# Kernel tuning notes

Hardware: AMD Instinct MI355X
Metric: run time of the kernel (lower is better)

The kernel has to match this reference:

```python
import jax, jax.numpy as jnp
import numpy as np

B, S, D, H, OUT = 512, 200, 64, 512, 1
EPS = 1e-5  # torch LayerNorm default


def ln(x, g, b, axes=-1):
    m = x.mean(axis=axes, keepdims=True)
    v = ((x - m) ** 2).mean(axis=axes, keepdims=True)
    return (x - m) * jax.lax.rsqrt(v + EPS) * g + b


def lstm_layer(xs, W_ih, b_ih, W_hh, b_hh, g_ih, be_ih, g_hh, be_hh, g_ho, be_ho):
    # xs: (S, B, in_dim) -> (S, B, H)
    nb = xs.shape[1]
    def step(carry, x_t):
        h, c = carry
        gates = ln(x_t @ W_ih.T + b_ih, g_ih, be_ih) + ln(h @ W_hh.T + b_hh, g_hh, be_hh)
        i, f, g, o = jnp.split(gates, 4, axis=-1)
        c_new = jax.nn.sigmoid(f) * c + jax.nn.sigmoid(i) * jnp.tanh(g)
        h_new = jax.nn.sigmoid(o) * ln(jnp.tanh(c_new), g_ho, be_ho)
        return (h_new, c_new), h_new
    init = (jnp.zeros((nb, H), xs.dtype), jnp.zeros((nb, H), xs.dtype))
    _, hs = jax.lax.scan(step, init, xs)
    return hs


def setup_inputs() -> dict:
    key = jax.random.key(0)
    ks = iter(jax.random.split(key, 16))
    scale = 0.02
    def rn(shape):
        return jax.random.normal(next(ks), shape, jnp.float32) * scale
    inp = {"x": jax.random.normal(next(ks), (B, S, D), jnp.float32)}
    inp["ln1_g"] = jnp.ones((S, D), jnp.float32)
    inp["ln1_b"] = jnp.zeros((S, D), jnp.float32)
    for l, ind in ((0, D), (1, H)):
        inp[f"W_ih{l}"] = rn((4 * H, ind)); inp[f"b_ih{l}"] = jnp.zeros((4 * H,), jnp.float32)
        inp[f"W_hh{l}"] = rn((4 * H, H));  inp[f"b_hh{l}"] = jnp.zeros((4 * H,), jnp.float32)
        inp[f"g_ih{l}"] = jnp.ones((4 * H,), jnp.float32); inp[f"be_ih{l}"] = jnp.zeros((4 * H,), jnp.float32)
        inp[f"g_hh{l}"] = jnp.ones((4 * H,), jnp.float32); inp[f"be_hh{l}"] = jnp.zeros((4 * H,), jnp.float32)
        inp[f"g_ho{l}"] = jnp.ones((H,), jnp.float32);     inp[f"be_ho{l}"] = jnp.zeros((H,), jnp.float32)
    inp["Wd1"] = rn((H // 4, H));      inp["bd1"] = jnp.zeros((H // 4,), jnp.float32)
    inp["Wd2"] = rn((H // 8, H // 4)); inp["bd2"] = jnp.zeros((H // 8,), jnp.float32)
    inp["Wd3"] = rn((H // 16, H // 8)); inp["bd3"] = jnp.zeros((H // 16,), jnp.float32)
    inp["Wd4"] = rn((OUT, H // 16));   inp["bd4"] = jnp.zeros((OUT,), jnp.float32)
    return inp


def _forward(x, ln1_g, ln1_b,
             W_ih0, b_ih0, W_hh0, b_hh0, g_ih0, be_ih0, g_hh0, be_hh0, g_ho0, be_ho0,
             W_ih1, b_ih1, W_hh1, b_hh1, g_ih1, be_ih1, g_hh1, be_hh1, g_ho1, be_ho1,
             Wd1, bd1, Wd2, bd2, Wd3, bd3, Wd4, bd4):
    # ln1 normalizes jointly over (seq_len, input_dim)
    x = ln(x, ln1_g, ln1_b, axes=(-2, -1))
    xs = jnp.transpose(x, (1, 0, 2))  # (S, B, D)
    hs = lstm_layer(xs, W_ih0, b_ih0, W_hh0, b_hh0, g_ih0, be_ih0, g_hh0, be_hh0, g_ho0, be_ho0)
    hs = lstm_layer(hs, W_ih1, b_ih1, W_hh1, b_hh1, g_ih1, be_ih1, g_hh1, be_hh1, g_ho1, be_ho1)
    h_last = hs[-1]  # (B, H): last_num=1, eval-mode dropout is identity
    z = jax.nn.relu(h_last @ Wd1.T + bd1)
    z = jax.nn.relu(z @ Wd2.T + bd2)
    z = jax.nn.relu(z @ Wd3.T + bd3)
    return z @ Wd4.T + bd4  # (B, OUT)


def reference(x, ln1_g, ln1_b,
              W_ih0, b_ih0, W_hh0, b_hh0, g_ih0, be_ih0, g_hh0, be_hh0, g_ho0, be_ho0,
              W_ih1, b_ih1, W_hh1, b_hh1, g_ih1, be_ih1, g_hh1, be_hh1, g_ho1, be_ho1,
              Wd1, bd1, Wd2, bd2, Wd3, bd3, Wd4, bd4):
    return _forward(x, ln1_g, ln1_b,
                    W_ih0, b_ih0, W_hh0, b_hh0, g_ih0, be_ih0, g_hh0, be_hh0, g_ho0, be_ho0,
                    W_ih1, b_ih1, W_hh1, b_hh1, g_ih1, be_ih1, g_hh1, be_hh1, g_ho1, be_ho1,
                    Wd1, bd1, Wd2, bd2, Wd3, bd3, Wd4, bd4)
```

## Files before the change

### kernel.cpp

```cpp
#include <hip/hip_runtime.h>
#include <math.h>

#define BATCH 512
#define SEQ   200
#define DIN   64
#define HID   512
#define GW    2048
#define EPS   1e-5f
#define NREG  4

typedef _Float16 half_t;
typedef half_t half8 __attribute__((ext_vector_type(8)));
typedef float  f32x4  __attribute__((ext_vector_type(4)));
typedef float  f32x16 __attribute__((ext_vector_type(16)));

#define WN0 (2048*64)
#define WN1 (2048*512)
#define WTOT (WN0 + 3*WN1)
#define XFRAG ((size_t)SEQ*16*4*512)

__device__ __forceinline__ float sigf(float x){ return 1.0f/(1.0f+expf(-x)); }

__device__ __forceinline__ void block_reduce4(float&a,float&b,float&c,float&d,float* red){
  #pragma unroll
  for(int o=32;o;o>>=1){
    a+=__shfl_down(a,o); b+=__shfl_down(b,o);
    c+=__shfl_down(c,o); d+=__shfl_down(d,o);
  }
  const int lane = threadIdx.x & 63, wid = threadIdx.x>>6;
  if(lane==0){ red[wid*4+0]=a; red[wid*4+1]=b; red[wid*4+2]=c; red[wid*4+3]=d; }
  __syncthreads();
  a = red[0]+red[4]+red[8]+red[12];
  b = red[1]+red[5]+red[9]+red[13];
  c = red[2]+red[6]+red[10]+red[14];
  d = red[3]+red[7]+red[11]+red[15];
  __syncthreads();
}

__global__ __launch_bounds__(256) void ln1_stats(const float* __restrict__ x,
                                                 float* __restrict__ mu,
                                                 float* __restrict__ rs){
  const int b = blockIdx.x;
  const float* xb = x + (size_t)b*SEQ*DIN;
  float s=0, ss=0, d=0, e=0;
  for (int i=threadIdx.x; i<SEQ*DIN; i+=256){ float v=xb[i]; s+=v; ss+=v*v; }
  __shared__ float red[16];
  block_reduce4(s,ss,d,e,red);
  if (threadIdx.x==0){
    float m = s*(1.0f/(SEQ*DIN));
    mu[b] = m;
    rs[b] = rsqrtf(ss*(1.0f/(SEQ*DIN)) - m*m + EPS);
  }
}

__global__ __launch_bounds__(256) void wsplit(
    const float* __restrict__ W0, const float* __restrict__ W1,
    const float* __restrict__ W2, const float* __restrict__ W3,
    half_t* __restrict__ Wh, half_t* __restrict__ Wl)
{
  int i = blockIdx.x*256 + threadIdx.x;
  if (i >= WTOT) return;
  const float* src; int off, Kd;
  if (i < WN0){ src=W0; off=i; Kd=DIN; }
  else {
    int r = (i-WN0)/WN1; off = (i-WN0) - r*WN1; Kd=HID;
    src = (r==0)?W1:((r==1)?W2:W3);
  }
  const int C = Kd>>5;
  int j  = off & 7;
  int l  = (off>>3) & 63;
  int ks = (off>>9) & 1;
  int nf = (off>>10) & 1;
  int pc = off>>11;
  int c  = pc & (C-1);
  int p  = pc >> (Kd==DIN ? 1 : 4);
  int n  = p*64 + nf*32 + (l&31);
  int k  = c*32 + ks*16 + (l>>5)*8 + j;
  float v = src[(size_t)n*Kd + k];
  half_t h = (half_t)v;
  Wh[i] = h;
  Wl[i] = (half_t)(v - (float)h);
}

__global__ __launch_bounds__(256) void xprep(
    const float* __restrict__ x, const float* __restrict__ g1, const float* __restrict__ b1,
    const float* __restrict__ mu, const float* __restrict__ rs,
    half_t* __restrict__ xh, half_t* __restrict__ xl)
{
  size_t i = (size_t)blockIdx.x*256 + threadIdx.x;
  if (i >= XFRAG) return;
  int j   = (int)(i & 7);
  int l   = (int)((i>>3) & 63);
  int c   = (int)((i>>9) & 3);
  int mch = (int)((i>>11) & 15);
  int t   = (int)(i>>15);
  int b   = mch*32 + (l&31);
  int k   = c*16 + ((l>>5)<<3) + j;
  float v = (x[(size_t)b*(SEQ*DIN) + t*DIN + k] - mu[b]) * rs[b]
            * g1[t*DIN+k] + b1[t*DIN+k];
  half_t h = (half_t)v;
  xh[i] = h;
  xl[i] = (half_t)(v - (float)h);
}

__global__ __launch_bounds__(256, 1) void tick_mm64(
    const half_t* __restrict__ xh, const half_t* __restrict__ xl,
    const half_t* __restrict__ h0fh, const half_t* __restrict__ h0fl,
    const half_t* __restrict__ h1fh, const half_t* __restrict__ h1fl,
    const half_t* __restrict__ Wh, const half_t* __restrict__ Wl,
    float* __restrict__ G, int t)
{
  const int z    = blockIdx.z;
  const int tid  = threadIdx.x;
  const int lane = tid & 63;
  const int w    = tid >> 6;
  const int ln31 = lane & 31;

  const int mch0 = blockIdx.y*2;
  const int p    = blockIdx.x*4 + w;
  const int wn0  = p*64;

  const half_t* Bh = Wh + WN0; const half_t* Bl = Wl + WN0;
  int Kd = HID;
  if (z==0){ Bh=Wh; Bl=Wl; Kd=DIN; }
  else if (z==2){ Bh=Wh+WN0+WN1; Bl=Wl+WN0+WN1; }
  else if (z==3){ Bh=Wh+WN0+2*WN1; Bl=Wl+WN0+2*WN1; }

  const int C32 = Kd >> 5;
  const int C16 = Kd >> 4;

  const half_t* Bph = Bh + (size_t)p*C32*2048 + lane*8;
  const half_t* Bpl = Bl + (size_t)p*C32*2048 + lane*8;

  const int tq = (t < SEQ) ? t : (SEQ-1);
  const half_t *Aph0,*Apl0,*Aph1,*Apl1;
  if (z==0){
    const size_t xb = ((size_t)tq*16 + mch0)*2048 + lane*8;
    Aph0 = xh + xb; Aph1 = xh + xb + 2048;
    Apl0 = xl + xb; Apl1 = xl + xb + 2048;
  } else {
    const half_t* FAh = (z==3) ? h1fh : h0fh;
    const half_t* FAl = (z==3) ? h1fl : h0fl;
    const size_t ab = (size_t)mch0*16384 + lane*8;
    Aph0 = FAh + ab; Aph1 = FAh + ab + 16384;
    Apl0 = FAl + ab; Apl1 = FAl + ab + 16384;
  }

  f32x16 acc00 = {0.f,0.f,0.f,0.f,0.f,0.f,0.f,0.f,0.f,0.f,0.f,0.f,0.f,0.f,0.f,0.f};
  f32x16 acc01 = acc00, acc10 = acc00, acc11 = acc00;

  struct F { half8 ah0,al0,ah1,al1,bh0,bh1,bl0,bl1; };
  auto loadF = [&](int c)->F{
    F f;
    const size_t ao = (size_t)c*512;
    f.ah0 = *(const half8*)(Aph0 + ao);
    f.al0 = *(const half8*)(Apl0 + ao);
    f.ah1 = *(const half8*)(Aph1 + ao);
    f.al1 = *(const half8*)(Apl1 + ao);
    const size_t bo = (size_t)(c>>1)*2048 + (size_t)(c&1)*512;
    f.bh0 = *(const half8*)(Bph + bo);
    f.bh1 = *(const half8*)(Bph + bo + 1024);
    f.bl0 = *(const half8*)(Bpl + bo);
    f.bl1 = *(const half8*)(Bpl + bo + 1024);
    return f;
  };
  auto mmstep = [&](const F& f){
    acc00 = __builtin_amdgcn_mfma_f32_32x32x16_f16(f.ah0, f.bh0, acc00, 0,0,0);
    acc01 = __builtin_amdgcn_mfma_f32_32x32x16_f16(f.ah0, f.bh1, acc01, 0,0,0);
    acc10 = __builtin_amdgcn_mfma_f32_32x32x16_f16(f.ah1, f.bh0, acc10, 0,0,0);
    acc11 = __builtin_amdgcn_mfma_f32_32x32x16_f16(f.ah1, f.bh1, acc11, 0,0,0);
    acc00 = __builtin_amdgcn_mfma_f32_32x32x16_f16(f.al0, f.bh0, acc00, 0,0,0);
    acc01 = __builtin_amdgcn_mfma_f32_32x32x16_f16(f.al0, f.bh1, acc01, 0,0,0);
    acc10 = __builtin_amdgcn_mfma_f32_32x32x16_f16(f.al1, f.bh0, acc10, 0,0,0);
    acc11 = __builtin_amdgcn_mfma_f32_32x32x16_f16(f.al1, f.bh1, acc11, 0,0,0);
    acc00 = __builtin_amdgcn_mfma_f32_32x32x16_f16(f.ah0, f.bl0, acc00, 0,0,0);
    acc01 = __builtin_amdgcn_mfma_f32_32x32x16_f16(f.ah0, f.bl1, acc01, 0,0,0);
    acc10 = __builtin_amdgcn_mfma_f32_32x32x16_f16(f.ah1, f.bl0, acc10, 0,0,0);
    acc11 = __builtin_amdgcn_mfma_f32_32x32x16_f16(f.ah1, f.bl1, acc11, 0,0,0);
  };

  F f0 = loadF(0);
  F f1 = loadF(1);
  for (int c=0; c<C16; c+=2){
    F f2, f3;
    if (c+2 < C16){ f2 = loadF(c+2); f3 = loadF(c+3); }
    mmstep(f0);
    mmstep(f1);
    f0 = f2; f1 = f3;
  }

  float* Gr = G + (size_t)z*BATCH*GW;
  const int rbase = (lane>>5)<<2;
  #pragma unroll
  for (int reg=0; reg<16; reg++){
    const int row = (reg&3) + ((reg>>2)<<3) + rbase;
    const int m0 = mch0*32 + row;
    const int m1 = m0 + 32;
    __builtin_nontemporal_store(acc00[reg], &Gr[(size_t)m0*GW + wn0 + ln31]);
    __builtin_nontemporal_store(acc01[reg], &Gr[(size_t)m0*GW + wn0 + 32 + ln31]);
    __builtin_nontemporal_store(acc10[reg], &Gr[(size_t)m1*GW + wn0 + ln31]);
    __builtin_nontemporal_store(acc11[reg], &Gr[(size_t)m1*GW + wn0 + 32 + ln31]);
  }
}

__global__ __launch_bounds__(256) void tick_update(
    const float* __restrict__ G,
    const float* __restrict__ b_ih0, const float* __restrict__ b_hh0,
    const float* __restrict__ b_ih1, const float* __restrict__ b_hh1,
    const float* __restrict__ g_ih0, const float* __restrict__ be_ih0,
    const float* __restrict__ g_hh0, const float* __restrict__ be_hh0,
    const float* __restrict__ g_ho0, const float* __restrict__ be_ho0,
    const float* __restrict__ g_ih1, const float* __restrict__ be_ih1,
    const float* __restrict__ g_hh1, const float* __restrict__ be_hh1,
    const float* __restrict__ g_ho1, const float* __restrict__ be_ho1,
    float* __restrict__ h0, float* __restrict__ c0,
    float* __restrict__ h1, float* __restrict__ c1,
    half_t* __restrict__ h0fh, half_t* __restrict__ h0fl,
    half_t* __restrict__ h1fh, half_t* __restrict__ h1fl, int t)
{
  const int layer = blockIdx.x >> 9;
  const int b = blockIdx.x & 511;
  if (layer==0 && t>=SEQ) return;
  if (layer==1 && t==0)   return;

  const float *GA,*GB,*bA,*bB,*gA,*beA,*gB,*beB,*gH,*bH;
  float *cs,*hs; half_t *hfx,*lfx;
  const size_t rb = (size_t)b*GW;
  if (layer==0){
    GA = G + rb;
    GB = G + (size_t)1*BATCH*GW + rb;
    bA=b_ih0; bB=b_hh0;
    gA=g_ih0; beA=be_ih0; gB=g_hh0; beB=be_hh0; gH=g_ho0; bH=be_ho0;
    cs = c0 + b*HID; hs = h0 + b*HID; hfx = h0fh; lfx = h0fl;
  } else {
    GA = G + (size_t)2*BATCH*GW + rb;
    GB = G + (size_t)3*BATCH*GW + rb;
    bA=b_ih1; bB=b_hh1;
    gA=g_ih1; beA=be_ih1; gB=g_hh1; beB=be_hh1; gH=g_ho1; bH=be_ho1;
    cs = c1 + b*HID; hs = h1 + b*HID; hfx = h1fh; lfx = h1fl;
  }

  const int tid = threadIdx.x;
  __shared__ float red[16];
  __shared__ __align__(16) float GS[2*GW];
  __shared__ float su[HID];
  __shared__ float so[HID];

  float sa=0, ssa=0, sb=0, ssb=0;
  for (int i=tid*4; i<GW; i+=1024){
    f32x4 va = *(const f32x4*)(GA+i);
    va += *(const f32x4*)(bA+i);
    *(f32x4*)(GS+i) = va;
    f32x4 vb = *(const f32x4*)(GB+i);
    vb += *(const f32x4*)(bB+i);
    *(f32x4*)(GS+GW+i) = vb;
    #pragma unroll
    for (int q=0;q<4;q++){
      sa += va[q]; ssa += va[q]*va[q];
      sb += vb[q]; ssb += vb[q]*vb[q];
    }
  }
  block_reduce4(sa,ssa,sb,ssb,red);
  const float ma = sa*(1.0f/GW);
  const float ra = rsqrtf(ssa*(1.0f/GW) - ma*ma + EPS);
  const float mb = sb*(1.0f/GW);
  const float rb_ = rsqrtf(ssb*(1.0f/GW) - mb*mb + EPS);

  float s_u=0, s_uu=0;
  for (int j=tid;j<HID;j+=256){
    float iv = ((GS[j      ]-ma)*ra*gA[j      ]+beA[j      ]) + ((GS[GW+j      ]-mb)*rb_*gB[j      ]+beB[j      ]);
    float fv = ((GS[j+  HID]-ma)*ra*gA[j+  HID]+beA[j+  HID]) + ((GS[GW+j+  HID]-mb)*rb_*gB[j+  HID]+beB[j+  HID]);
    float gv = ((GS[j+2*HID]-ma)*ra*gA[j+2*HID]+beA[j+2*HID]) + ((GS[GW+j+2*HID]-mb)*rb_*gB[j+2*HID]+beB[j+2*HID]);
    float ov = ((GS[j+3*HID]-ma)*ra*gA[j+3*HID]+beA[j+3*HID]) + ((GS[GW+j+3*HID]-mb)*rb_*gB[j+3*HID]+beB[j+3*HID]);
    float cn = sigf(fv)*cs[j] + sigf(iv)*tanhf(gv);
    cs[j] = cn;
    float u = tanhf(cn);
    su[j] = u; so[j] = sigf(ov);
    s_u += u; s_uu += u*u;
  }
  float d3=0,d4=0;
  block_reduce4(s_u,s_uu,d3,d4,red);
  const float mu_u = s_u*(1.0f/HID);
  const float ru   = rsqrtf(s_uu*(1.0f/HID) - mu_u*mu_u + EPS);

  const size_t fbase = ((size_t)(b>>5)*32)*512 + (size_t)(b&31)*8;
  for (int j=tid;j<HID;j+=256){
    float v = so[j] * ((su[j]-mu_u)*ru*gH[j] + bH[j]);
    hs[j] = v;
    half_t hv = (half_t)v;
    half_t lv = (half_t)(v - (float)hv);
    const size_t fi = fbase + (size_t)(j>>4)*512 + (size_t)((j>>3)&1)*256 + (j&7);
    hfx[fi] = hv;
    lfx[fi] = lv;
  }
}

__global__ __launch_bounds__(256) void head_kernel(
    const float* __restrict__ h1,
    const float* __restrict__ Wd1, const float* __restrict__ bd1,
    const float* __restrict__ Wd2, const float* __restrict__ bd2,
    const float* __restrict__ Wd3, const float* __restrict__ bd3,
    const float* __restrict__ Wd4, const float* __restrict__ bd4,
    float* __restrict__ out)
{
  const int b = blockIdx.x;
  __shared__ float hv[HID];
  __shared__ float z1[128];
  __shared__ float z2[64];
  __shared__ float z3[32];
  const int tid = threadIdx.x;
  for (int i=tid;i<HID;i+=256) hv[i]=h1[(size_t)b*HID+i];
  __syncthreads();
  if (tid<128){
    float acc=bd1[tid]; const float* w=Wd1+(size_t)tid*512;
    for(int k=0;k<512;k++) acc+=hv[k]*w[k];
    z1[tid]=fmaxf(acc,0.f);
  }
  __syncthreads();
  if (tid<64){
    float acc=bd2[tid]; const float* w=Wd2+(size_t)tid*128;
    for(int k=0;k<128;k++) acc+=z1[k]*w[k];
    z2[tid]=fmaxf(acc,0.f);
  }
  __syncthreads();
  if (tid<32){
    float acc=bd3[tid]; const float* w=Wd3+(size_t)tid*64;
    for(int k=0;k<64;k++) acc+=z2[k]*w[k];
    z3[tid]=fmaxf(acc,0.f);
  }
  __syncthreads();
  if (tid==0){
    float acc=bd4[0];
    for(int k=0;k<32;k++) acc+=z3[k]*Wd4[k];
    out[b]=acc;
  }
}

extern "C" void kernel_launch(void* const* d_in, const int* in_sizes, int n_in,
                              void* d_out, int out_size, void* d_ws, size_t ws_size,
                              hipStream_t stream) {
  const float* x      = (const float*)d_in[0];
  const float* ln1_g  = (const float*)d_in[1];
  const float* ln1_b  = (const float*)d_in[2];
  const float* W_ih0  = (const float*)d_in[3];
  const float* b_ih0  = (const float*)d_in[4];
  const float* W_hh0  = (const float*)d_in[5];
  const float* b_hh0  = (const float*)d_in[6];
  const float* g_ih0  = (const float*)d_in[7];
  const float* be_ih0 = (const float*)d_in[8];
  const float* g_hh0  = (const float*)d_in[9];
  const float* be_hh0 = (const float*)d_in[10];
  const float* g_ho0  = (const float*)d_in[11];
  const float* be_ho0 = (const float*)d_in[12];
  const float* W_ih1  = (const float*)d_in[13];
  const float* b_ih1  = (const float*)d_in[14];
  const float* W_hh1  = (const float*)d_in[15];
  const float* b_hh1  = (const float*)d_in[16];
  const float* g_ih1  = (const float*)d_in[17];
  const float* be_ih1 = (const float*)d_in[18];
  const float* g_hh1  = (const float*)d_in[19];
  const float* be_hh1 = (const float*)d_in[20];
  const float* g_ho1  = (const float*)d_in[21];
  const float* be_ho1 = (const float*)d_in[22];
  const float* Wd1    = (const float*)d_in[23];
  const float* bd1    = (const float*)d_in[24];
  const float* Wd2    = (const float*)d_in[25];
  const float* bd2    = (const float*)d_in[26];
  const float* Wd3    = (const float*)d_in[27];
  const float* bd3    = (const float*)d_in[28];
  const float* Wd4    = (const float*)d_in[29];
  const float* bd4    = (const float*)d_in[30];
  float* out = (float*)d_out;

  float* ws = (float*)d_ws;
  float* G  = ws;
  float* h0 = G  + NREG*(size_t)BATCH*GW;
  float* c0 = h0 + (size_t)BATCH*HID;
  float* h1 = c0 + (size_t)BATCH*HID;
  float* c1 = h1 + (size_t)BATCH*HID;
  half_t* h0fh = (half_t*)(c1 + (size_t)BATCH*HID);
  half_t* h0fl = h0fh + (size_t)BATCH*HID;
  half_t* h1fh = h0fl + (size_t)BATCH*HID;
  half_t* h1fl = h1fh + (size_t)BATCH*HID;
  float* mu = (float*)(h1fl + (size_t)BATCH*HID);
  float* rs = mu + BATCH;
  half_t* Wh = (half_t*)(rs + BATCH);
  half_t* Wl = Wh + (size_t)WTOT;
  half_t* xh = Wl + (size_t)WTOT;
  half_t* xl = xh + XFRAG;

  hipMemsetAsync(h0, 0, 4*(size_t)BATCH*HID*4 + 4*(size_t)BATCH*HID*2, stream);

  ln1_stats<<<BATCH, 256, 0, stream>>>(x, mu, rs);
  wsplit<<<(WTOT+255)/256, 256, 0, stream>>>(W_ih0, W_hh0, W_ih1, W_hh1, Wh, Wl);
  xprep<<<(int)((XFRAG+255)/256), 256, 0, stream>>>(x, ln1_g, ln1_b, mu, rs, xh, xl);

  dim3 mgrid(8, 8, NREG);
  for (int t = 0; t <= SEQ; ++t) {
    tick_mm64<<<mgrid, 256, 0, stream>>>(xh, xl,
        h0fh, h0fl, h1fh, h1fl, Wh, Wl, G, t);
    tick_update<<<dim3(1024), 256, 0, stream>>>(G,
        b_ih0, b_hh0, b_ih1, b_hh1,
        g_ih0, be_ih0, g_hh0, be_hh0, g_ho0, be_ho0,
        g_ih1, be_ih1, g_hh1, be_hh1, g_ho1, be_ho1,
        h0, c0, h1, c1, h0fh, h0fl, h1fh, h1fl, t);
  }
  head_kernel<<<BATCH, 256, 0, stream>>>(h1, Wd1, bd1, Wd2, bd2, Wd3, bd3, Wd4, bd4, out);
}
```

Before: 5.677 ms.

## Fuse matmul and update phases into staggered combined kernels with double-buffered h0

The per-tick matmul and LSTM-update kernels are merged into a single 'phase' kernel that runs matmul blocks for one layer alongside update blocks for the other layer, skewing the two layers in time. Layer-0 hidden fragments are double-buffered by parity so layer-1 matmuls can read the previous h0 while layer-0 updates write the next. This puts GEMM and elementwise work in the same launch so they can share the GPU, at the cost of 640-block launches, a different dependency schedule and extra buffers. G reads also switch to nontemporal loads.

New measurement: 7.288 ms. 28.4% more time.

```diff
diff --git a/kernel.cpp b/kernel.cpp
--- a/kernel.cpp
+++ b/kernel.cpp
@@ -18,6 +18,7 @@
 #define WN1 (2048*512)
 #define WTOT (WN0 + 3*WN1)
 #define XFRAG ((size_t)SEQ*16*4*512)
+#define HFRAG ((size_t)BATCH*HID)
 
 __device__ __forceinline__ float sigf(float x){ return 1.0f/(1.0f+expf(-x)); }
 
@@ -103,21 +104,21 @@
   xl[i] = (half_t)(v - (float)h);
 }
 
-__global__ __launch_bounds__(256, 1) void tick_mm64(
+__device__ __forceinline__ void mm_block(
+    int z, int q, int t,
     const half_t* __restrict__ xh, const half_t* __restrict__ xl,
     const half_t* __restrict__ h0fh, const half_t* __restrict__ h0fl,
     const half_t* __restrict__ h1fh, const half_t* __restrict__ h1fl,
     const half_t* __restrict__ Wh, const half_t* __restrict__ Wl,
-    float* __restrict__ G, int t)
-{
-  const int z    = blockIdx.z;
+    float* __restrict__ G)
+{
   const int tid  = threadIdx.x;
   const int lane = tid & 63;
   const int w    = tid >> 6;
   const int ln31 = lane & 31;
 
-  const int mch0 = blockIdx.y*2;
-  const int p    = blockIdx.x*4 + w;
+  const int mch0 = (q>>3)*2;
+  const int p    = (q&7)*4 + w;
   const int wn0  = p*64;
 
   const half_t* Bh = Wh + WN0; const half_t* Bl = Wl + WN0;
@@ -132,15 +133,18 @@
   const half_t* Bph = Bh + (size_t)p*C32*2048 + lane*8;
   const half_t* Bpl = Bl + (size_t)p*C32*2048 + lane*8;
 
-  const int tq = (t < SEQ) ? t : (SEQ-1);
   const half_t *Aph0,*Apl0,*Aph1,*Apl1;
   if (z==0){
-    const size_t xb = ((size_t)tq*16 + mch0)*2048 + lane*8;
+    const size_t xb = ((size_t)t*16 + mch0)*2048 + lane*8;
     Aph0 = xh + xb; Aph1 = xh + xb + 2048;
     Apl0 = xl + xb; Apl1 = xl + xb + 2048;
   } else {
-    const half_t* FAh = (z==3) ? h1fh : h0fh;
-    const half_t* FAl = (z==3) ? h1fl : h0fl;
+    const half_t *FAh, *FAl;
+    if (z==3){ FAh = h1fh; FAl = h1fl; }
+    else {
+      const size_t par = (size_t)((t-1)&1)*HFRAG;
+      FAh = h0fh + par; FAl = h0fl + par;
+    }
     const size_t ab = (size_t)mch0*16384 + lane*8;
     Aph0 = FAh + ab; Aph1 = FAh + ab + 16384;
     Apl0 = FAl + ab; Apl1 = FAl + ab + 16384;
@@ -203,7 +207,8 @@
   }
 }
 
-__global__ __launch_bounds__(256) void tick_update(
+__device__ __forceinline__ void upd_unit(
+    int layer, int b, int s,
     const float* __restrict__ G,
     const float* __restrict__ b_ih0, const float* __restrict__ b_hh0,
     const float* __restrict__ b_ih1, const float* __restrict__ b_hh1,
@@ -213,25 +218,22 @@
     const float* __restrict__ g_ih1, const float* __restrict__ be_ih1,
     const float* __restrict__ g_hh1, const float* __restrict__ be_hh1,
     const float* __restrict__ g_ho1, const float* __restrict__ be_ho1,
-    float* __restrict__ h0, float* __restrict__ c0,
-    float* __restrict__ h1, float* __restrict__ c1,
+    float* __restrict__ c0, float* __restrict__ c1, float* __restrict__ h1,
     half_t* __restrict__ h0fh, half_t* __restrict__ h0fl,
-    half_t* __restrict__ h1fh, half_t* __restrict__ h1fl, int t)
-{
-  const int layer = blockIdx.x >> 9;
-  const int b = blockIdx.x & 511;
-  if (layer==0 && t>=SEQ) return;
-  if (layer==1 && t==0)   return;
-
+    half_t* __restrict__ h1fh, half_t* __restrict__ h1fl,
+    float* GS, float* red)
+{
   const float *GA,*GB,*bA,*bB,*gA,*beA,*gB,*beB,*gH,*bH;
-  float *cs,*hs; half_t *hfx,*lfx;
+  float *cs, *hs=nullptr; half_t *hfx,*lfx;
   const size_t rb = (size_t)b*GW;
   if (layer==0){
     GA = G + rb;
     GB = G + (size_t)1*BATCH*GW + rb;
     bA=b_ih0; bB=b_hh0;
     gA=g_ih0; beA=be_ih0; gB=g_hh0; beB=be_hh0; gH=g_ho0; bH=be_ho0;
-    cs = c0 + b*HID; hs = h0 + b*HID; hfx = h0fh; lfx = h0fl;
+    cs = c0 + b*HID;
+    const size_t par = (size_t)(s&1)*HFRAG;
+    hfx = h0fh + par; lfx = h0fl + par;
   } else {
     GA = G + (size_t)2*BATCH*GW + rb;
     GB = G + (size_t)3*BATCH*GW + rb;
@@ -241,17 +243,15 @@
   }
 
   const int tid = threadIdx.x;
-  __shared__ float red[16];
-  __shared__ __align__(16) float GS[2*GW];
   __shared__ float su[HID];
   __shared__ float so[HID];
 
   float sa=0, ssa=0, sb=0, ssb=0;
   for (int i=tid*4; i<GW; i+=1024){
-    f32x4 va = *(const f32x4*)(GA+i);
+    f32x4 va = __builtin_nontemporal_load((const f32x4*)(GA+i));
     va += *(const f32x4*)(bA+i);
     *(f32x4*)(GS+i) = va;
-    f32x4 vb = *(const f32x4*)(GB+i);
+    f32x4 vb = __builtin_nontemporal_load((const f32x4*)(GB+i));
     vb += *(const f32x4*)(bB+i);
     *(f32x4*)(GS+GW+i) = vb;
     #pragma unroll
@@ -286,12 +286,50 @@
   const size_t fbase = ((size_t)(b>>5)*32)*512 + (size_t)(b&31)*8;
   for (int j=tid;j<HID;j+=256){
     float v = so[j] * ((su[j]-mu_u)*ru*gH[j] + bH[j]);
-    hs[j] = v;
+    if (hs) hs[j] = v;
     half_t hv = (half_t)v;
     half_t lv = (half_t)(v - (float)hv);
     const size_t fi = fbase + (size_t)(j>>4)*512 + (size_t)((j>>3)&1)*256 + (j&7);
     hfx[fi] = hv;
     lfx[fi] = lv;
+  }
+}
+
+__global__ __launch_bounds__(256, 2) void phase(
+    int mode, int t,
+    const half_t* __restrict__ xh, const half_t* __restrict__ xl,
+    half_t* __restrict__ h0fh, half_t* __restrict__ h0fl,
+    half_t* __restrict__ h1fh, half_t* __restrict__ h1fl,
+    const half_t* __restrict__ Wh, const half_t* __restrict__ Wl,
+    float* __restrict__ G,
+    const float* __restrict__ b_ih0, const float* __restrict__ b_hh0,
+    const float* __restrict__ b_ih1, const float* __restrict__ b_hh1,
+    const float* __restrict__ g_ih0, const float* __restrict__ be_ih0,
+    const float* __restrict__ g_hh0, const float* __restrict__ be_hh0,
+    const float* __restrict__ g_ho0, const float* __restrict__ be_ho0,
+    const float* __restrict__ g_ih1, const float* __restrict__ be_ih1,
+    const float* __restrict__ g_hh1, const float* __restrict__ be_hh1,
+    const float* __restrict__ g_ho1, const float* __restrict__ be_ho1,
+    float* __restrict__ c0, float* __restrict__ c1, float* __restrict__ h1)
+{
+  __shared__ __align__(16) float GS[2*GW];
+  __shared__ float red[16];
+  const int bi = blockIdx.x;
+  if (bi < 128){
+    if (mode==0){ if (t > 199) return; }
+    else        { if (t < 1 || t > 200) return; }
+    const int z = (mode==0 ? 0 : 2) + (bi>>6);
+    mm_block(z, bi&63, t, xh, xl, h0fh, h0fl, h1fh, h1fl, Wh, Wl, G);
+  } else {
+    const int b = bi - 128;
+    const int layer = (mode==0) ? 1 : 0;
+    const int s     = (mode==0) ? t-2 : t;
+    if (s < 0 || s > 199) return;
+    upd_unit(layer, b, s, G,
+             b_ih0, b_hh0, b_ih1, b_hh1,
+             g_ih0, be_ih0, g_hh0, be_hh0, g_ho0, be_ho0,
+             g_ih1, be_ih1, g_hh1, be_hh1, g_ho1, be_ho1,
+             c0, c1, h1, h0fh, h0fl, h1fh, h1fl, GS, red);
   }
 }
 
@@ -374,36 +412,40 @@
 
   float* ws = (float*)d_ws;
   float* G  = ws;
-  float* h0 = G  + NREG*(size_t)BATCH*GW;
-  float* c0 = h0 + (size_t)BATCH*HID;
-  float* h1 = c0 + (size_t)BATCH*HID;
-  float* c1 = h1 + (size_t)BATCH*HID;
-  half_t* h0fh = (half_t*)(c1 + (size_t)BATCH*HID);
-  half_t* h0fl = h0fh + (size_t)BATCH*HID;
-  half_t* h1fh = h0fl + (size_t)BATCH*HID;
-  half_t* h1fl = h1fh + (size_t)BATCH*HID;
-  float* mu = (float*)(h1fl + (size_t)BATCH*HID);
+  float* c0 = G  + NREG*(size_t)BATCH*GW;
+  float* c1 = c0 + (size_t)BATCH*HID;
+  float* h1 = c1 + (size_t)BATCH*HID;
+  half_t* h0fh = (half_t*)(h1 + (size_t)BATCH*HID);
+  half_t* h0fl = h0fh + 2*HFRAG;
+  half_t* h1fh = h0fl + 2*HFRAG;
+  half_t* h1fl = h1fh + HFRAG;
+  float* mu = (float*)(h1fl + HFRAG);
   float* rs = mu + BATCH;
   half_t* Wh = (half_t*)(rs + BATCH);
   half_t* Wl = Wh + (size_t)WTOT;
   half_t* xh = Wl + (size_t)WTOT;
   half_t* xl = xh + XFRAG;
 
-  hipMemsetAsync(h0, 0, 4*(size_t)BATCH*HID*4 + 4*(size_t)BATCH*HID*2, stream);
+  (void)hipMemsetAsync(c0, 0, 3*(size_t)BATCH*HID*4 + 6*HFRAG*2, stream);
 
   ln1_stats<<<BATCH, 256, 0, stream>>>(x, mu, rs);
   wsplit<<<(WTOT+255)/256, 256, 0, stream>>>(W_ih0, W_hh0, W_ih1, W_hh1, Wh, Wl);
   xprep<<<(int)((XFRAG+255)/256), 256, 0, stream>>>(x, ln1_g, ln1_b, mu, rs, xh, xl);
 
-  dim3 mgrid(8, 8, NREG);
-  for (int t = 0; t <= SEQ; ++t) {
-    tick_mm64<<<mgrid, 256, 0, stream>>>(xh, xl,
-        h0fh, h0fl, h1fh, h1fl, Wh, Wl, G, t);
-    tick_update<<<dim3(1024), 256, 0, stream>>>(G,
+  for (int t = 0; t <= 201; ++t) {
+    phase<<<640, 256, 0, stream>>>(0, t,
+        xh, xl, h0fh, h0fl, h1fh, h1fl, Wh, Wl, G,
         b_ih0, b_hh0, b_ih1, b_hh1,
         g_ih0, be_ih0, g_hh0, be_hh0, g_ho0, be_ho0,
         g_ih1, be_ih1, g_hh1, be_hh1, g_ho1, be_ho1,
-        h0, c0, h1, c1, h0fh, h0fl, h1fh, h1fl, t);
+        c0, c1, h1);
+    if (t <= 200)
+      phase<<<640, 256, 0, stream>>>(1, t,
+          xh, xl, h0fh, h0fl, h1fh, h1fl, Wh, Wl, G,
+          b_ih0, b_hh0, b_ih1, b_hh1,
+          g_ih0, be_ih0, g_hh0, be_hh0, g_ho0, be_ho0,
+          g_ih1, be_ih1, g_hh1, be_hh1, g_ho1, be_ho1,
+          c0, c1, h1);
   }
   head_kernel<<<BATCH, 256, 0, stream>>>(h1, Wd1, bd1, Wd2, bd2, Wd3, bd3, Wd4, bd4, out);
 }
```
